# Optimization experiments

Hardware: AMD Instinct MI355X
Metric: run time of the kernel (lower is better)

The kernel has to match this reference:

```python
import jax, jax.numpy as jnp
import numpy as np

H = 16      # n_head
DK = 64     # d_k = n_feat // n_head
EPS = 1e-5  # nn.LayerNorm default eps


def _layernorm(x, gamma, beta):
    # LayerNorm over the last (d_k) dim, matching nn.LayerNorm(d_k)
    mu = jnp.mean(x, axis=-1, keepdims=True)
    var = jnp.mean(jnp.square(x - mu), axis=-1, keepdims=True)
    return (x - mu) * jax.lax.rsqrt(var + EPS) * gamma + beta


def setup_inputs() -> dict:
    key = jax.random.key(0)
    ks = jax.random.split(key, 10)
    B, T, D = 4, 1024, 1024
    s = 0.02
    inp = {
        "query": jax.random.normal(ks[0], (B, T, D), dtype=jnp.float32),
        "key":   jax.random.normal(ks[1], (B, T, D), dtype=jnp.float32),
        "value": jax.random.normal(ks[2], (B, T, D), dtype=jnp.float32),
        "mask":  jax.random.randint(ks[3], (B, T, T), 0, 2).astype(bool),
        # projection weights (torch nn.Linear: y = x @ W.T + b)
        "Wq": jax.random.normal(ks[4], (D, D), dtype=jnp.float32) * s,
        "bq": jnp.zeros((D,), dtype=jnp.float32),
        "Wk": jax.random.normal(ks[5], (D, D), dtype=jnp.float32) * s,
        "bk": jnp.zeros((D,), dtype=jnp.float32),
        "Wv": jax.random.normal(ks[6], (D, D), dtype=jnp.float32) * s,
        "bv": jnp.zeros((D,), dtype=jnp.float32),
        "Wo": jax.random.normal(ks[7], (D, D), dtype=jnp.float32) * s,
        "bo": jnp.zeros((D,), dtype=jnp.float32),
        # per-head LayerNorm params over d_k
        "q_gamma": jnp.ones((DK,), dtype=jnp.float32),
        "q_beta":  jnp.zeros((DK,), dtype=jnp.float32),
        "k_gamma": jnp.ones((DK,), dtype=jnp.float32),
        "k_beta":  jnp.zeros((DK,), dtype=jnp.float32),
    }
    return inp


def reference(query, key, value, mask, Wq, bq, Wk, bk, Wv, bv, Wo, bo,
              q_gamma, q_beta, k_gamma, k_beta):
    B, Tq, D = query.shape
    Tk = key.shape[1]
    # forward_qkv: project, split heads, QK-LayerNorm
    q = (query @ Wq.T + bq).reshape(B, Tq, H, DK)
    k = (key   @ Wk.T + bk).reshape(B, Tk, H, DK)
    q = _layernorm(q, q_gamma, q_beta).transpose(0, 2, 1, 3)  # (B,H,Tq,dk)
    k = _layernorm(k, k_gamma, k_beta).transpose(0, 2, 1, 3)  # (B,H,Tk,dk)
    v = (value @ Wv.T + bv).reshape(B, Tk, H, DK).transpose(0, 2, 1, 3)
    # scores scaled by sqrt(d_k)
    scores = jnp.einsum('bhqd,bhkd->bhqk', q, k) / jnp.sqrt(jnp.float32(DK))
    m = mask[:, None]  # (B,1,Tq,Tk) broadcast over heads
    scores = jnp.where(m, jnp.float32(-10000.0), scores)
    attn = jax.nn.softmax(scores, axis=-1)
    attn = jnp.where(m, jnp.float32(0.0), attn)
    # dropout is identity (p=0.0, eval)
    x = jnp.einsum('bhqk,bhkd->bhqd', attn, v)
    x = x.transpose(0, 2, 1, 3).reshape(B, Tq, H * DK)
    return x @ Wo.T + bo
```

## Files before the change

### kernel.cpp

```cpp
#include <hip/hip_runtime.h>
#include <cstdint>
#include <cstddef>

typedef _Float16 half8  __attribute__((ext_vector_type(8)));
typedef _Float16 half4v __attribute__((ext_vector_type(4)));
typedef float    f32x4  __attribute__((ext_vector_type(4)));

__device__ __forceinline__ f32x4 fzero4() {
  f32x4 v; v[0] = v[1] = v[2] = v[3] = 0.0f; return v;
}

__device__ __forceinline__ void gload16(const void* g, void* l) {
  __builtin_amdgcn_global_load_lds(
      (const __attribute__((address_space(1))) unsigned int*)g,
      (__attribute__((address_space(3))) unsigned int*)l, 16, 0, 0);
}

#define MFMA(a, b, c) __builtin_amdgcn_mfma_f32_16x16x32_f16(a, b, c, 0, 0, 0)
#define EXP2(x) __builtin_amdgcn_exp2f(x)

__device__ __forceinline__ float row16_sum(float x) {
#define STEP_(N)                                                         \
  {                                                                      \
    int t_ = __builtin_amdgcn_update_dpp(0, __float_as_int(x), 0x120 | N, \
                                         0xf, 0xf, true);                \
    x = x + __int_as_float(t_);                                          \
  }
  STEP_(8) STEP_(4) STEP_(2) STEP_(1)
#undef STEP_
  return x;
}

struct PrepArgs {
  const float* wsrc[4];
  _Float16*    wdst[4];
  const int*   mask;
  unsigned long long* mbits;
};

__global__ __launch_bounds__(256) void prep_kernel(PrepArgs a) {
  const int z = blockIdx.y;
  const int nthr = gridDim.x * blockDim.x;
  const int t0 = blockIdx.x * blockDim.x + threadIdx.x;
  if (z < 4) {
    const float4* __restrict__ s = (const float4*)a.wsrc[z];
    half4v* __restrict__ d = (half4v*)a.wdst[z];
    float4 v[2];
#pragma unroll
    for (int k = 0; k < 2; ++k) v[k] = s[t0 + k * nthr];
#pragma unroll
    for (int k = 0; k < 2; ++k) {
      half4v h;
      h[0] = (_Float16)v[k].x; h[1] = (_Float16)v[k].y;
      h[2] = (_Float16)v[k].z; h[3] = (_Float16)v[k].w;
      d[t0 + k * nthr] = h;
    }
  } else {
    const int* __restrict__ src = a.mask;
    const unsigned char* __restrict__ s8 = (const unsigned char*)src;
    unsigned long long* __restrict__ dst = a.mbits;
    const int lane = threadIdx.x & 63;
    unsigned probe = 0;
#pragma unroll
    for (int e = 0; e < 16; ++e) probe |= s8[4 * (lane * 16 + e) + 1];
    const bool isbool = __any(probe != 0);

    const int gw = blockIdx.x * 4 + (threadIdx.x >> 6);
    for (int ii = 0; ii < 32; ii += 8) {
      int mv[8];
#pragma unroll
      for (int k = 0; k < 8; ++k) {
        const int word = gw * 32 + ii + k;
        const int t = word & 1023;
        const int kw = (word >> 10) & 15;
        const int b = word >> 14;
        const size_t idx = ((size_t)(b * 1024 + t)) * 1024 + kw * 64 + lane;
        mv[k] = isbool ? (int)s8[idx] : src[idx];
      }
#pragma unroll
      for (int k = 0; k < 8; ++k) {
        unsigned long long bal = __ballot(mv[k] != 0);
        if (lane == 0) dst[gw * 32 + ii + k] = bal;
      }
    }
  }
}

#define SM_SCALE 0.18033688011112042f

__global__ __launch_bounds__(256) void proj_kernel(
    const float* __restrict__ query, const float* __restrict__ key,
    const float* __restrict__ value, const _Float16* __restrict__ w16,
    const float* __restrict__ bq, const float* __restrict__ bk,
    const float* __restrict__ bv,
    const float* __restrict__ qg, const float* __restrict__ qbt,
    const float* __restrict__ kg, const float* __restrict__ kbt,
    _Float16* __restrict__ Qln, _Float16* __restrict__ Kln,
    _Float16* __restrict__ VT) {
  __shared__ _Float16 As[2][128 * 64];
  __shared__ _Float16 Bs[2][128 * 64];

  const int tid = threadIdx.x;
  const int w = tid >> 6, lane = tid & 63, g = lane >> 4, l15 = lane & 15;
  const int flat = blockIdx.x;
  const int swz = (flat & 7) * 96 + (flat >> 3);
  const int bn = swz & 7;
  const int bm = (swz >> 3) & 31;
  const int z = swz >> 8;

  const float* Af = (z == 0) ? query : ((z == 1) ? key : value);
  const _Float16* W = w16 + (size_t)z * (1024 * 1024);
  const float* bias = (z == 0) ? bq : ((z == 1) ? bk : bv);

  const int wr = w >> 1, wc = w & 1;
  const int srow = (w << 3) + (lane >> 3);
  const int csw = ((lane & 7) ^ (lane >> 3)) << 3;
  const int rsw = (l15 & 7) << 3;

  const int arow0 = tid >> 3;
  const int acg = tid & 7;
  const int axor = ((acg ^ (arow0 & 7)) << 3);

  f32x4 acc[4][4];
#pragma unroll
  for (int i = 0; i < 4; ++i)
#pragma unroll
    for (int j = 0; j < 4; ++j) acc[i][j] = fzero4();

  float4 va[4][2];

#define PROJ_LOADA(KT)                                                      \
  _Pragma("unroll") for (int s_ = 0; s_ < 4; ++s_) {                        \
    const float4* ap_ = (const float4*)(Af +                                \
        (size_t)(bm * 128 + s_ * 32 + arow0) * 1024 + (KT)*64 + acg * 8);   \
    va[s_][0] = ap_[0];                                                     \
    va[s_][1] = ap_[1];                                                     \
  }

#define PROJ_WRITEA(BUF)                                                    \
  _Pragma("unroll") for (int s_ = 0; s_ < 4; ++s_) {                        \
    half8 h_;                                                               \
    h_[0] = (_Float16)va[s_][0].x; h_[1] = (_Float16)va[s_][0].y;           \
    h_[2] = (_Float16)va[s_][0].z; h_[3] = (_Float16)va[s_][0].w;           \
    h_[4] = (_Float16)va[s_][1].x; h_[5] = (_Float16)va[s_][1].y;           \
    h_[6] = (_Float16)va[s_][1].z; h_[7] = (_Float16)va[s_][1].w;           \
    *(half8*)&As[BUF][(s_ * 32 + arow0) * 64 + axor] = h_;                  \
  }

#define PROJ_STAGEB(KT, BUF)                                                \
  _Pragma("unroll") for (int r = 0; r < 4; ++r) {                           \
    gload16(W + (size_t)(bn * 128 + r * 32 + srow) * 1024 + (KT)*64 + csw,  \
            &Bs[BUF][(r * 32 + (w << 3)) * 64]);                            \
  }

#define PROJ_TILE(KT, CUR, NXT, PF)                                         \
  {                                                                         \
    if (PF) { PROJ_LOADA((KT) + 1) PROJ_STAGEB((KT) + 1, NXT) }             \
    _Pragma("unroll") for (int kk = 0; kk < 2; ++kk) {                      \
      half8 a[4], b[4];                                                     \
      _Pragma("unroll") for (int mi = 0; mi < 4; ++mi) a[mi] =              \
          *(const half8*)&As[CUR][(wr * 64 + mi * 16 + l15) * 64 +          \
                                  ((kk * 32 + g * 8) ^ rsw)];               \
      _Pragma("unroll") for (int nj = 0; nj < 4; ++nj) b[nj] =              \
          *(const half8*)&Bs[CUR][(wc * 64 + nj * 16 + l15) * 64 +          \
                                  ((kk * 32 + g * 8) ^ rsw)];               \
      __builtin_amdgcn_s_setprio(1);                                        \
      _Pragma("unroll") for (int mi = 0; mi < 4; ++mi)                      \
          _Pragma("unroll") for (int nj = 0; nj < 4; ++nj) acc[mi][nj] =    \
              MFMA(a[mi], b[nj], acc[mi][nj]);                              \
      __builtin_amdgcn_s_setprio(0);                                        \
    }                                                                       \
    if (PF) {                                                               \
      asm volatile("s_waitcnt vmcnt(0)" ::: "memory");                      \
      PROJ_WRITEA(NXT)                                                      \
      __syncthreads();                                                      \
    }                                                                       \
  }

  PROJ_LOADA(0)
  PROJ_STAGEB(0, 0)
  asm volatile("s_waitcnt vmcnt(0)" ::: "memory");
  PROJ_WRITEA(0)
  __syncthreads();
  for (int kt = 0; kt < 16; kt += 2) {
    PROJ_TILE(kt, 0, 1, true);
    PROJ_TILE(kt + 1, 1, 0, (kt + 1) < 15);
  }
#undef PROJ_TILE
#undef PROJ_STAGEB
#undef PROJ_WRITEA
#undef PROJ_LOADA

  const int colbase = bn * 128 + wc * 64;
  const int h = colbase >> 6;
  const int rowbase = bm * 128 + wr * 64;

  float biasv[4];
#pragma unroll
  for (int nj = 0; nj < 4; ++nj) biasv[nj] = bias[colbase + nj * 16 + l15];

  if (z < 2) {
    const float* gamma = (z == 0) ? qg : kg;
    const float* beta = (z == 0) ? qbt : kbt;
    const float sc = (z == 0) ? SM_SCALE : 1.0f;
    _Float16* dst = (z == 0) ? Qln : Kln;
    float gam[4], bet[4];
#pragma unroll
    for (int nj = 0; nj < 4; ++nj) {
      gam[nj] = gamma[nj * 16 + l15] * sc;
      bet[nj] = beta[nj * 16 + l15] * sc;
    }
#pragma unroll
    for (int mi = 0; mi < 4; ++mi) {
#pragma unroll
      for (int j = 0; j < 4; ++j) {
        float vals[4], s = 0.f, s2 = 0.f;
#pragma unroll
        for (int nj = 0; nj < 4; ++nj) {
          float v = acc[mi][nj][j] + biasv[nj];
          vals[nj] = v; s += v; s2 += v * v;
        }
        s = row16_sum(s);
        s2 = row16_sum(s2);
        const float mu = s * (1.0f / 64.0f);
        const float var = s2 * (1.0f / 64.0f) - mu * mu;
        const float rs = rsqrtf(var + 1e-5f);
        const int r = rowbase + mi * 16 + g * 4 + j;
        const int b = r >> 10, t = r & 1023;
        _Float16* drow = dst + ((size_t)((b * 16 + h) * 1024 + t)) * 64;
#pragma unroll
        for (int nj = 0; nj < 4; ++nj)
          drow[nj * 16 + l15] =
              (_Float16)((vals[nj] - mu) * rs * gam[nj] + bet[nj]);
      }
    }
  } else {
#pragma unroll
    for (int mi = 0; mi < 4; ++mi) {
      const int r0 = rowbase + mi * 16 + g * 4;
      const int b = r0 >> 10, t0 = r0 & 1023;
#pragma unroll
      for (int nj = 0; nj < 4; ++nj) {
        const int dk = nj * 16 + l15;
        half4v pk;
#pragma unroll
        for (int j = 0; j < 4; ++j)
          pk[j] = (_Float16)(acc[mi][nj][j] + biasv[nj]);
        *(half4v*)&VT[((size_t)((b * 16 + h) * 64 + dk)) * 1024 + t0] = pk;
      }
    }
  }
}

#define PSTR 76

__global__ __launch_bounds__(512) void attn_kernel(
    const _Float16* __restrict__ Qln, const _Float16* __restrict__ Kln,
    const _Float16* __restrict__ VT,
    const unsigned long long* __restrict__ mbits, _Float16* __restrict__ X) {
  __shared__ _Float16 PQ[128 * PSTR];
  __shared__ _Float16 Ks[2][64 * 64];
  __shared__ _Float16 Vs[2][64 * 64];
  __shared__ unsigned long long Mb[2][128];

  const int tid = threadIdx.x;
  const int w = tid >> 6, lane = tid & 63, g = lane >> 4, l15 = lane & 15;
  const int qt = blockIdx.y;
  const int bh = blockIdx.x;
  const int b = bh >> 4, h = bh & 15;

  const int lr8 = lane >> 3;
  const int csw = ((lane & 7) ^ lr8) << 3;

  const _Float16* Qb = Qln + (size_t)bh * 65536;
  const _Float16* Kb = Kln + (size_t)bh * 65536;
  const _Float16* Vb = VT + (size_t)bh * 65536;
  const unsigned long long* mbb = mbits + (size_t)b * 16384 + qt * 128;

  gload16(Qb + (size_t)(qt * 128 + w * 16 + lr8) * 64 + csw, &PQ[(w * 16) * 64]);
  gload16(Qb + (size_t)(qt * 128 + w * 16 + 8 + lr8) * 64 + csw,
          &PQ[(w * 16 + 8) * 64]);
  gload16(Kb + (size_t)(w * 8 + lr8) * 64 + csw, &Ks[0][(w * 8) * 64]);
  gload16(Vb + (size_t)(w * 8 + lr8) * 1024 + csw, &Vs[0][(w * 8) * 64]);
  if (w == 0) gload16(mbb + lane * 2, &Mb[0][0]);
  asm volatile("s_waitcnt vmcnt(0)" ::: "memory");
  __syncthreads();

  const int rsw = (l15 & 7) << 3;
  half8 qf[2];
#pragma unroll
  for (int kk = 0; kk < 2; ++kk)
    qf[kk] = *(const half8*)&PQ[(w * 16 + l15) * 64 + ((kk * 32 + g * 8) ^ rsw)];
  asm volatile("s_waitcnt lgkmcnt(0)" ::: "memory");
  __syncthreads();

  f32x4 o[4];
  float lsum[4];
#pragma unroll
  for (int dn = 0; dn < 4; ++dn) o[dn] = fzero4();
#pragma unroll
  for (int j = 0; j < 4; ++j) lsum[j] = 0.f;

#define ATTN_TILE(KT, CUR, NXT, PF)                                          \
  {                                                                          \
    if (PF) {                                                                \
      gload16(Kb + (size_t)(((KT) + 1) * 64 + w * 8 + lr8) * 64 + csw,       \
              &Ks[NXT][(w * 8) * 64]);                                       \
      gload16(Vb + (size_t)(w * 8 + lr8) * 1024 + ((KT) + 1) * 64 + csw,     \
              &Vs[NXT][(w * 8) * 64]);                                       \
      if (w == 0)                                                            \
        gload16(mbb + (size_t)((KT) + 1) * 1024 + lane * 2, &Mb[NXT][0]);    \
    }                                                                        \
    f32x4 s[4];                                                              \
    _Pragma("unroll") for (int nj = 0; nj < 4; ++nj) s[nj] = fzero4();       \
    _Pragma("unroll") for (int kk = 0; kk < 2; ++kk) {                       \
      half8 qv = qf[kk];                                                     \
      __builtin_amdgcn_s_setprio(1);                                         \
      _Pragma("unroll") for (int nj = 0; nj < 4; ++nj) {                     \
        half8 kf = *(const half8*)&Ks[CUR][(nj * 16 + l15) * 64 +            \
                                          ((kk * 32 + g * 8) ^ rsw)];        \
        s[nj] = MFMA(qv, kf, s[nj]);                                         \
      }                                                                      \
      __builtin_amdgcn_s_setprio(0);                                         \
    }                                                                        \
    _Pragma("unroll") for (int j = 0; j < 4; ++j) {                          \
      const int lrow = w * 16 + g * 4 + j;                                   \
      const unsigned long long mw = Mb[CUR][lrow];                           \
      const unsigned lo = (unsigned)mw, hi = (unsigned)(mw >> 32);           \
      const float p0 = ((lo >> l15) & 1) ? 0.f : EXP2(s[0][j]);              \
      const float p1 = ((lo >> (l15 + 16)) & 1) ? 0.f : EXP2(s[1][j]);       \
      const float p2 = ((hi >> l15) & 1) ? 0.f : EXP2(s[2][j]);              \
      const float p3 = ((hi >> (l15 + 16)) & 1) ? 0.f : EXP2(s[3][j]);       \
      PQ[lrow * PSTR + 0 + l15] = (_Float16)p0;                              \
      PQ[lrow * PSTR + 16 + l15] = (_Float16)p1;                             \
      PQ[lrow * PSTR + 32 + l15] = (_Float16)p2;                             \
      PQ[lrow * PSTR + 48 + l15] = (_Float16)p3;                             \
      lsum[j] += (p0 + p1) + (p2 + p3);                                      \
    }                                                                        \
    _Pragma("unroll") for (int kk = 0; kk < 2; ++kk) {                       \
      half8 pa = *(const half8*)&PQ[(w * 16 + l15) * PSTR + kk * 32 + g * 8];\
      __builtin_amdgcn_s_setprio(1);                                         \
      _Pragma("unroll") for (int dn = 0; dn < 4; ++dn) {                     \
        half8 vf = *(const half8*)&Vs[CUR][(dn * 16 + l15) * 64 +            \
                                           ((kk * 32 + g * 8) ^ rsw)];       \
        o[dn] = MFMA(pa, vf, o[dn]);                                         \
      }                                                                      \
      __builtin_amdgcn_s_setprio(0);                                         \
    }                                                                        \
    if (PF) {                                                                \
      asm volatile("s_waitcnt vmcnt(0)" ::: "memory");                       \
      __syncthreads();                                                       \
    }                                                                        \
  }

  for (int kt = 0; kt < 16; kt += 2) {
    ATTN_TILE(kt, 0, 1, true);
    ATTN_TILE(kt + 1, 1, 0, (kt + 1) < 15);
  }
#undef ATTN_TILE

#pragma unroll
  for (int j = 0; j < 4; ++j) {
    const int t = qt * 128 + w * 16 + g * 4 + j;
    const float inv = 1.0f / row16_sum(lsum[j]);
    _Float16* xrow = X + ((size_t)(b * 1024 + t)) * 1024 + h * 64;
#pragma unroll
    for (int dn = 0; dn < 4; ++dn)
      xrow[dn * 16 + l15] = (_Float16)(o[dn][j] * inv);
  }
}

__global__ __launch_bounds__(256) void ogemm_kernel(
    const _Float16* __restrict__ Xin, const _Float16* __restrict__ Wo16,
    const float* __restrict__ bo, float* __restrict__ out) {
  __shared__ _Float16 As[2][128 * 64];
  __shared__ _Float16 Bs[2][64 * 64];

  const int tid = threadIdx.x;
  const int w = tid >> 6, lane = tid & 63, g = lane >> 4, l15 = lane & 15;
  const int flat = blockIdx.x;
  const int swz = (flat & 7) * 64 + (flat >> 3);
  const int bn = swz & 15;
  const int bm = swz >> 4;
  const int wr = w >> 1, wc = w & 1;
  const int srow = (w << 3) + (lane >> 3);
  const int lr8 = lane >> 3;
  const int csw = ((lane & 7) ^ lr8) << 3;
  const int rsw = (l15 & 7) << 3;

  f32x4 acc[4][2];
#pragma unroll
  for (int i = 0; i < 4; ++i)
#pragma unroll
    for (int j = 0; j < 2; ++j) acc[i][j] = fzero4();

#define OG_STAGE(KT, BUF)                                                   \
  {                                                                         \
    _Pragma("unroll") for (int r = 0; r < 4; ++r) {                         \
      gload16(Xin + (size_t)(bm * 128 + r * 32 + srow) * 1024 + (KT)*64 +   \
                  csw,                                                      \
              &As[BUF][(r * 32 + (w << 3)) * 64]);                          \
    }                                                                       \
    _Pragma("unroll") for (int c = 0; c < 2; ++c) {                         \
      gload16(Wo16 + (size_t)(bn * 64 + w * 16 + c * 8 + lr8) * 1024 +      \
                  (KT)*64 + csw,                                            \
              &Bs[BUF][(w * 16 + c * 8) * 64]);                             \
    }                                                                       \
  }

#define OG_TILE(KT, CUR, NXT, PF)                                           \
  {                                                                         \
    if (PF) { OG_STAGE((KT) + 1, NXT) }                                     \
    _Pragma("unroll") for (int kk = 0; kk < 2; ++kk) {                      \
      half8 a[4], b[2];                                                     \
      _Pragma("unroll") for (int mi = 0; mi < 4; ++mi) a[mi] =              \
          *(const half8*)&As[CUR][(wr * 64 + mi * 16 + l15) * 64 +          \
                                  ((kk * 32 + g * 8) ^ rsw)];               \
      _Pragma("unroll") for (int nj = 0; nj < 2; ++nj) b[nj] =              \
          *(const half8*)&Bs[CUR][(wc * 32 + nj * 16 + l15) * 64 +          \
                                  ((kk * 32 + g * 8) ^ rsw)];               \
      __builtin_amdgcn_s_setprio(1);                                        \
      _Pragma("unroll") for (int mi = 0; mi < 4; ++mi)                      \
          _Pragma("unroll") for (int nj = 0; nj < 2; ++nj) acc[mi][nj] =    \
              MFMA(a[mi], b[nj], acc[mi][nj]);                              \
      __builtin_amdgcn_s_setprio(0);                                        \
    }                                                                       \
    if (PF) {                                                               \
      asm volatile("s_waitcnt vmcnt(0)" ::: "memory");                      \
      __syncthreads();                                                      \
    }                                                                       \
  }

  OG_STAGE(0, 0)
  asm volatile("s_waitcnt vmcnt(0)" ::: "memory");
  __syncthreads();
  for (int kt = 0; kt < 16; kt += 2) {
    OG_TILE(kt, 0, 1, true);
    OG_TILE(kt + 1, 1, 0, (kt + 1) < 15);
  }
#undef OG_TILE
#undef OG_STAGE

  const int colbase = bn * 64 + wc * 32;
  const int rowbase = bm * 128 + wr * 64;
  float biasv[2];
#pragma unroll
  for (int nj = 0; nj < 2; ++nj) biasv[nj] = bo[colbase + nj * 16 + l15];
#pragma unroll
  for (int mi = 0; mi < 4; ++mi)
#pragma unroll
    for (int nj = 0; nj < 2; ++nj)
#pragma unroll
      for (int j = 0; j < 4; ++j) {
        const int r = rowbase + mi * 16 + g * 4 + j;
        out[(size_t)r * 1024 + colbase + nj * 16 + l15] =
            acc[mi][nj][j] + biasv[nj];
      }
}

extern "C" void kernel_launch(void* const* d_in, const int* in_sizes, int n_in,
                              void* d_out, int out_size, void* d_ws,
                              size_t ws_size, hipStream_t stream) {
  const float* query = (const float*)d_in[0];
  const float* key = (const float*)d_in[1];
  const float* value = (const float*)d_in[2];
  const int* mask = (const int*)d_in[3];
  const float* Wq = (const float*)d_in[4];
  const float* bq = (const float*)d_in[5];
  const float* Wk = (const float*)d_in[6];
  const float* bk = (const float*)d_in[7];
  const float* Wv = (const float*)d_in[8];
  const float* bv = (const float*)d_in[9];
  const float* Wo = (const float*)d_in[10];
  const float* bo = (const float*)d_in[11];
  const float* qg = (const float*)d_in[12];
  const float* qb = (const float*)d_in[13];
  const float* kg = (const float*)d_in[14];
  const float* kb = (const float*)d_in[15];
  float* out = (float*)d_out;

  const size_t M4 = (size_t)4 * 1024 * 1024;
  const size_t M1 = (size_t)1024 * 1024;
  _Float16* base = (_Float16*)d_ws;
  _Float16* X = base;
  _Float16* w16 = base + 3 * M4;
  _Float16* Qln = base + 4 * M4;
  _Float16* Kln = base + 5 * M4;
  _Float16* VTp = base + 6 * M4;
  unsigned long long* mbits = (unsigned long long*)(base + 7 * M4);

  PrepArgs pa;
  pa.wsrc[0] = Wq; pa.wsrc[1] = Wk; pa.wsrc[2] = Wv; pa.wsrc[3] = Wo;
  pa.wdst[0] = w16; pa.wdst[1] = w16 + M1; pa.wdst[2] = w16 + 2 * M1;
  pa.wdst[3] = w16 + 3 * M1;
  pa.mask = mask;
  pa.mbits = mbits;

  prep_kernel<<<dim3(512, 5), 256, 0, stream>>>(pa);
  proj_kernel<<<dim3(768), 256, 0, stream>>>(
      query, key, value, w16, bq, bk, bv, qg, qb, kg, kb, Qln, Kln, VTp);
  attn_kernel<<<dim3(64, 8), 512, 0, stream>>>(Qln, Kln, VTp, mbits, X);
  ogemm_kernel<<<dim3(512), 256, 0, stream>>>(X, w16 + 3 * M1, bo, out);
}
```

Baseline: 119.5 us.

## Single-buffer projection GEMM LDS tiles to cut shared memory footprint

Replaces the double-buffered A/B LDS tiles in the QKV projection kernel with single buffers, halving shared memory from 64KB to 32KB per block. The loop now stages B, writes A, issues the next A global load, syncs, computes, and syncs again. Lower LDS use may let more blocks reside per CU, but B loads are no longer overlapped with compute and there are two barriers per k-tile.

```diff
diff --git a/kernel.cpp b/kernel.cpp
--- a/kernel.cpp
+++ b/kernel.cpp
@@ -97,8 +97,8 @@
     const float* __restrict__ kg, const float* __restrict__ kbt,
     _Float16* __restrict__ Qln, _Float16* __restrict__ Kln,
     _Float16* __restrict__ VT) {
-  __shared__ _Float16 As[2][128 * 64];
-  __shared__ _Float16 Bs[2][128 * 64];
+  __shared__ _Float16 As[128 * 64];
+  __shared__ _Float16 Bs[128 * 64];
 
   const int tid = threadIdx.x;
   const int w = tid >> 6, lane = tid & 63, g = lane >> 4, l15 = lane & 15;
@@ -137,56 +137,49 @@
     va[s_][1] = ap_[1];                                                     \
   }
 
-#define PROJ_WRITEA(BUF)                                                    \
+#define PROJ_WRITEA()                                                       \
   _Pragma("unroll") for (int s_ = 0; s_ < 4; ++s_) {                        \
     half8 h_;                                                               \
     h_[0] = (_Float16)va[s_][0].x; h_[1] = (_Float16)va[s_][0].y;           \
     h_[2] = (_Float16)va[s_][0].z; h_[3] = (_Float16)va[s_][0].w;           \
     h_[4] = (_Float16)va[s_][1].x; h_[5] = (_Float16)va[s_][1].y;           \
     h_[6] = (_Float16)va[s_][1].z; h_[7] = (_Float16)va[s_][1].w;           \
-    *(half8*)&As[BUF][(s_ * 32 + arow0) * 64 + axor] = h_;                  \
-  }
-
-#define PROJ_STAGEB(KT, BUF)                                                \
+    *(half8*)&As[(s_ * 32 + arow0) * 64 + axor] = h_;                       \
+  }
+
+#define PROJ_STAGEB(KT)                                                     \
   _Pragma("unroll") for (int r = 0; r < 4; ++r) {                           \
     gload16(W + (size_t)(bn * 128 + r * 32 + srow) * 1024 + (KT)*64 + csw,  \
-            &Bs[BUF][(r * 32 + (w << 3)) * 64]);                            \
-  }
-
-#define PROJ_TILE(KT, CUR, NXT, PF)                                         \
-  {                                                                         \
-    if (PF) { PROJ_LOADA((KT) + 1) PROJ_STAGEB((KT) + 1, NXT) }             \
-    _Pragma("unroll") for (int kk = 0; kk < 2; ++kk) {                      \
-      half8 a[4], b[4];                                                     \
-      _Pragma("unroll") for (int mi = 0; mi < 4; ++mi) a[mi] =              \
-          *(const half8*)&As[CUR][(wr * 64 + mi * 16 + l15) * 64 +          \
-                                  ((kk * 32 + g * 8) ^ rsw)];               \
-      _Pragma("unroll") for (int nj = 0; nj < 4; ++nj) b[nj] =              \
-          *(const half8*)&Bs[CUR][(wc * 64 + nj * 16 + l15) * 64 +          \
-                                  ((kk * 32 + g * 8) ^ rsw)];               \
-      __builtin_amdgcn_s_setprio(1);                                        \
-      _Pragma("unroll") for (int mi = 0; mi < 4; ++mi)                      \
-          _Pragma("unroll") for (int nj = 0; nj < 4; ++nj) acc[mi][nj] =    \
-              MFMA(a[mi], b[nj], acc[mi][nj]);                              \
-      __builtin_amdgcn_s_setprio(0);                                        \
-    }                                                                       \
-    if (PF) {                                                               \
-      asm volatile("s_waitcnt vmcnt(0)" ::: "memory");                      \
-      PROJ_WRITEA(NXT)                                                      \
-      __syncthreads();                                                      \
-    }                                                                       \
+            &Bs[(r * 32 + (w << 3)) * 64]);                                 \
+  }
+
+#define PROJ_COMP()                                                         \
+  _Pragma("unroll") for (int kk = 0; kk < 2; ++kk) {                        \
+    half8 a[4], b[4];                                                       \
+    _Pragma("unroll") for (int mi = 0; mi < 4; ++mi) a[mi] =                \
+        *(const half8*)&As[(wr * 64 + mi * 16 + l15) * 64 +                 \
+                           ((kk * 32 + g * 8) ^ rsw)];                      \
+    _Pragma("unroll") for (int nj = 0; nj < 4; ++nj) b[nj] =                \
+        *(const half8*)&Bs[(wc * 64 + nj * 16 + l15) * 64 +                 \
+                           ((kk * 32 + g * 8) ^ rsw)];                      \
+    __builtin_amdgcn_s_setprio(1);                                          \
+    _Pragma("unroll") for (int mi = 0; mi < 4; ++mi)                        \
+        _Pragma("unroll") for (int nj = 0; nj < 4; ++nj) acc[mi][nj] =      \
+            MFMA(a[mi], b[nj], acc[mi][nj]);                                \
+    __builtin_amdgcn_s_setprio(0);                                          \
   }
 
   PROJ_LOADA(0)
-  PROJ_STAGEB(0, 0)
-  asm volatile("s_waitcnt vmcnt(0)" ::: "memory");
-  PROJ_WRITEA(0)
-  __syncthreads();
-  for (int kt = 0; kt < 16; kt += 2) {
-    PROJ_TILE(kt, 0, 1, true);
-    PROJ_TILE(kt + 1, 1, 0, (kt + 1) < 15);
-  }
-#undef PROJ_TILE
+  for (int kt = 0; kt < 16; ++kt) {
+    PROJ_STAGEB(kt)
+    asm volatile("s_waitcnt vmcnt(0)" ::: "memory");
+    PROJ_WRITEA()
+    if (kt < 15) PROJ_LOADA(kt + 1)
+    __syncthreads();
+    PROJ_COMP()
+    __syncthreads();
+  }
+#undef PROJ_COMP
 #undef PROJ_STAGEB
 #undef PROJ_WRITEA
 #undef PROJ_LOADA
```

After: 136.1 us. 13.9% more time.
